# Optimization experiments

Measured on AMD Instinct MI355X. Metric: run time of the kernel, lower is better.

The kernel has to match this reference:

```python
import jax, jax.numpy as jnp
import numpy as np

T, B, E, H, R, NHASH, CHUNK = 2048, 2, 1024, 8, 2, 8, 32
D = E // H
INF = 1.0e16  # module's self.inf
BIG = 1.0e8   # module's self.big


def setup_inputs() -> dict:
    key = jax.random.key(0)
    ks = jax.random.split(key, 8)
    w = lambda k, shape, s=0.02: jax.random.normal(k, shape, dtype=jnp.float32) * s
    return {
        "query": jax.random.normal(ks[0], (T, B, E), jnp.float32),
        "key":   jax.random.normal(ks[1], (T, B, E), jnp.float32),
        "value": jax.random.normal(ks[2], (T, B, E), jnp.float32),
        "Wq": w(ks[3], (E, E)), "bq": jnp.zeros((E,), jnp.float32),
        "Wv": w(ks[4], (E, E)), "bv": jnp.zeros((E,), jnp.float32),
        "Wo": w(ks[5], (E, E)), "bo": jnp.zeros((E,), jnp.float32),
        "hash_w": w(ks[6], (R, H, D, NHASH // 2), 0.1),
    }


def _hashes(x_tbhd, hash_w):
    # einsum('ibnf,rnfh->ibrnh'), cat([lin,-lin]), argmax -> [T,B,R,H]
    lin = jnp.einsum('tbhd,rhdn->tbrhn', x_tbhd, hash_w)
    return jnp.argmax(jnp.concatenate([lin, -lin], axis=-1), axis=-1)


def _gather_t(x_bhtd, perm_brht):
    # gather along T with per-(b,r,h) permutation -> [B,R,H,T,D]
    Bb, Rr, Hh, Tt = perm_brht.shape
    Dd = x_bhtd.shape[-1]
    xb = jnp.broadcast_to(x_bhtd[:, None], (Bb, Rr, Hh, Tt, Dd))
    idx = jnp.broadcast_to(perm_brht[..., None], (Bb, Rr, Hh, Tt, Dd))
    return jnp.take_along_axis(xb, idx, axis=3)


def reference(query, key, value, Wq, bq, Wv, bv, Wo, bo, hash_w):
    del key  # share_kq=True (self-attention): keys are L2-normalized queries
    scaling = D ** -0.5
    qf = query @ Wq + bq                                    # [T,B,E]
    kf = qf / jnp.linalg.norm(qf, axis=-1, keepdims=True)   # F.normalize over embed dim
    vf = value @ Wv + bv
    q = qf.reshape(T, B, H, D) * scaling
    k = kf.reshape(T, B, H, D)
    v = vf.reshape(T, B, H, D)

    q_hash = _hashes(q, hash_w)                             # [T,B,R,H]
    k_hash = _hashes(k, hash_w)

    qh_t = jnp.transpose(q_hash, (1, 2, 3, 0))              # [B,R,H,T]
    kh_t = jnp.transpose(k_hash, (1, 2, 3, 0))
    p_q = jnp.argsort(qh_t, axis=-1)                        # stable sort by hash
    p_k = jnp.argsort(kh_t, axis=-1)
    inv_q = jnp.argsort(p_q, axis=-1)                       # sorted position of each token

    q_s = _gather_t(jnp.transpose(q, (1, 2, 0, 3)), p_q)    # [B,R,H,T,D]
    k_s = _gather_t(jnp.transpose(k, (1, 2, 0, 3)), p_k)
    v_s = _gather_t(jnp.transpose(v, (1, 2, 0, 3)), p_k)
    qh_s = jnp.take_along_axis(qh_t, p_q, axis=-1)
    kh_s = jnp.take_along_axis(kh_t, p_k, axis=-1)

    C = T // CHUNK
    M = 3 * CHUNK
    chunk = lambda x: x.reshape(x.shape[:3] + (C, CHUNK) + x.shape[4:])
    q_c, qh_c, qid_c = chunk(q_s), chunk(qh_s), chunk(p_q)
    k_c, v_c, kh_c, kid_c = chunk(k_s), chunk(v_s), chunk(kh_s), chunk(p_k)

    # each query chunk attends key chunks {c-1, c, c+1} (num_chunk_offsets=3, wraparound)
    blocks = lambda x: jnp.concatenate([jnp.roll(x, 1, axis=3), x, jnp.roll(x, -1, axis=3)], axis=4)
    kb, vb, khb, kidb = blocks(k_c), blocks(v_c), blocks(kh_c), blocks(kid_c)

    scores = jnp.einsum('brhcld,brhcmd->brhclm', q_c, kb)   # q pre-scaled by d^-0.5
    scores = scores - INF * (qh_c[..., :, None] != khb[..., None, :])   # mask_different_hashes
    scores = scores - BIG * (qid_c[..., :, None] == kidb[..., None, :]) # mask_current

    # cross-round duplicate counting: key ids attended per original query
    chunk_of = inv_q // CHUNK                               # [B,R,H,T]
    idx = jnp.broadcast_to(chunk_of[..., None], (B, R, H, T, M))
    A = jnp.take_along_axis(kidb, idx, axis=3)              # [B,R,H,T,M]
    dup = []
    for r in range(R):
        c = jnp.zeros((B, H, T, M), jnp.int32)
        for r2 in range(R):
            c = c + (A[:, r, :, :, :, None] == A[:, r2, :, :, None, :]).sum(-1, dtype=jnp.int32)
        dup.append(c)
    dup = jnp.stack(dup, axis=1)                            # [B,R,H,T,M]
    idx2 = jnp.broadcast_to(p_q[..., None], (B, R, H, T, M))
    dup_s = jnp.take_along_axis(dup, idx2, axis=3)          # sorted-query order
    scores = scores - jnp.log(dup_s.astype(scores.dtype)).reshape(scores.shape)

    z = jax.nn.logsumexp(scores, axis=-1)                   # [B,R,H,C,L]
    attn = jax.nn.softmax(scores, axis=-1)
    o = jnp.einsum('brhclm,brhcmd->brhcld', attn, vb).reshape(B, R, H, T, D)
    z = z.reshape(B, R, H, T)

    # scatter back to original token order
    idx3 = jnp.broadcast_to(inv_q[..., None], (B, R, H, T, D))
    o = jnp.take_along_axis(o, idx3, axis=3)
    z = jnp.take_along_axis(z, inv_q, axis=3)

    w = jax.nn.softmax(z, axis=1)                           # combine rounds by logsumexp weight
    out = (w[..., None] * o).sum(axis=1)                    # [B,H,T,D]
    out = jnp.transpose(out, (2, 0, 1, 3)).reshape(T, B, E)
    return out @ Wo + bo
```

## Files before the change

### kernel.cpp

```cpp
#include <hip/hip_runtime.h>

typedef unsigned short ushort_t;
typedef __bf16 bf16x8 __attribute__((ext_vector_type(8)));
typedef float f32x4 __attribute__((ext_vector_type(4)));

#define T_DIM 2048
#define B_DIM 2
#define E_DIM 1024
#define H_DIM 8
#define R_DIM 2
#define D_DIM 128
#define M_WIN 96
#define SCALING 0.08838834764831845f
#define LN2F 0.69314718055994530942f

__device__ __forceinline__ float bfu(unsigned u) {
  union { unsigned i; float f; } x; x.i = u << 16; return x.f;
}
__device__ __forceinline__ unsigned f2bf(float f) {
  union { float f; unsigned i; } x; x.f = f;
  unsigned r = x.i + 0x7fffu + ((x.i >> 16) & 1u);
  return r >> 16;
}
__device__ __forceinline__ void gl_lds16(const void* g, void* l) {
  __builtin_amdgcn_global_load_lds(
      (const __attribute__((address_space(1))) unsigned int*)g,
      (__attribute__((address_space(3))) unsigned int*)l, 16, 0, 0);
}

__global__ __launch_bounds__(256, 4) void prep2_kernel(
    const float* __restrict__ query, const float* __restrict__ value,
    const float* __restrict__ Wq, const float* __restrict__ Wv,
    const float* __restrict__ Wo, const float* __restrict__ bq,
    const float* __restrict__ hw,
    ushort_t* __restrict__ qh, ushort_t* __restrict__ vh,
    ushort_t* __restrict__ WqT, ushort_t* __restrict__ WvT,
    ushort_t* __restrict__ WoT, float* __restrict__ F,
    float* __restrict__ cvec, float* __restrict__ snorm)
{
  __shared__ float plds[4160];
  const int bid = blockIdx.x, tid = threadIdx.x;
  if (bid < 8192) {
    const float* src = (bid < 4096) ? query : value;
    ushort_t* dst = (bid < 4096) ? qh : vh;
    int i = ((bid & 4095) * 256 + tid) * 4;
    float4 x = *(const float4*)&src[i];
    uint2 oh;
    oh.x = f2bf(x.x) | (f2bf(x.y) << 16);
    oh.y = f2bf(x.z) | (f2bf(x.w) << 16);
    *(uint2*)&dst[i] = oh;
  } else if (bid < 8960) {
    int idx = bid - 8192;
    const float* in = (idx < 256) ? Wq : (idx < 512) ? Wv : Wo;
    ushort_t* hi = (idx < 256) ? WqT : (idx < 512) ? WvT : WoT;
    int tile = idx & 255;
    int n0 = (tile & 15) * 64, k0 = (tile >> 4) * 64;
    float (*t64)[65] = (float(*)[65])plds;
    const int tr = tid >> 4, tc4 = (tid & 15) * 4;
#pragma unroll
    for (int rr = 0; rr < 64; rr += 16)
      *(float4*)&t64[tr + rr][tc4] = *(const float4*)&in[(size_t)(k0 + tr + rr) * E_DIM + n0 + tc4];
    __syncthreads();
#pragma unroll
    for (int rr = 0; rr < 64; rr += 16) {
      int n = n0 + tr + rr;
      uint2 oh;
      oh.x = f2bf(t64[tc4 + 0][tr + rr]) | (f2bf(t64[tc4 + 1][tr + rr]) << 16);
      oh.y = f2bf(t64[tc4 + 2][tr + rr]) | (f2bf(t64[tc4 + 3][tr + rr]) << 16);
      *(uint2*)&hi[(size_t)n * E_DIM + k0 + tc4] = oh;
    }
  } else if (bid < 9024) {
    float* wl = plds;
    const int rh = (bid - 8960) & 15, h = rh & 7;
    const int e = ((bid - 8960) >> 4) * 256 + tid;
    for (int i = tid; i < 512; i += 256) wl[i] = hw[rh * 512 + i];
    __syncthreads();
    const float* wr = Wq + (size_t)e * E_DIM + h * D_DIM;
    float a0 = 0.f, a1 = 0.f, a2 = 0.f, a3 = 0.f;
#pragma unroll 2
    for (int d = 0; d < 128; d += 2) {
      float2 q2 = *(const float2*)&wr[d];
      float4 w0 = *(const float4*)&wl[d * 4];
      float4 w1 = *(const float4*)&wl[d * 4 + 4];
      a0 += q2.x * w0.x + q2.y * w1.x;
      a1 += q2.x * w0.y + q2.y * w1.y;
      a2 += q2.x * w0.z + q2.y * w1.z;
      a3 += q2.x * w0.w + q2.y * w1.w;
    }
    float4 o; o.x = a0; o.y = a1; o.z = a2; o.w = a3;
    *(float4*)&F[(size_t)e * 64 + rh * 4] = o;
    if ((bid - 8960) < 16 && tid < 4) {
      float acc = 0.f;
#pragma unroll 1
      for (int d = 0; d < 128; ++d) acc += bq[h * D_DIM + d] * wl[d * 4 + tid];
      cvec[rh * 4 + tid] = acc;
    }
  } else {
    float4 z4 = {0.f, 0.f, 0.f, 0.f};
#pragma unroll
    for (int i = 0; i < 4; ++i)
      *(float4*)&snorm[(i * 256 + tid) * 4] = z4;
  }
}

__global__ __launch_bounds__(256) void hashlin_kernel(const float* __restrict__ query,
                                                      const float* __restrict__ F,
                                                      const float* __restrict__ cvec,
                                                      int* __restrict__ hashb)
{
  __shared__ float As[32][17];
  __shared__ float Fs[32][64];
  const int tid = threadIdx.x;
  const int ty = tid >> 4, tx = tid & 15;
  const int r0 = blockIdx.x * 16;
  float acc0 = 0.f, acc1 = 0.f, acc2 = 0.f, acc3 = 0.f;
  for (int k0 = 0; k0 < E_DIM; k0 += 32) {
    __syncthreads();
    {
      int i = tid * 2, row = i >> 5, kk = i & 31;
      float2 a2 = *(const float2*)&query[(size_t)(r0 + row) * E_DIM + k0 + kk];
      As[kk][row] = a2.x; As[kk + 1][row] = a2.y;
    }
    {
      int i = tid * 8, kk = i >> 6, cc = i & 63;
      float4 f0 = *(const float4*)&F[(size_t)(k0 + kk) * 64 + cc];
      float4 f1 = *(const float4*)&F[(size_t)(k0 + kk) * 64 + cc + 4];
      *(float4*)&Fs[kk][cc] = f0;
      *(float4*)&Fs[kk][cc + 4] = f1;
    }
    __syncthreads();
#pragma unroll
    for (int kk = 0; kk < 32; ++kk) {
      float a = As[kk][ty];
      float4 f4 = *(const float4*)&Fs[kk][tx * 4];
      acc0 += a * f4.x; acc1 += a * f4.y; acc2 += a * f4.z; acc3 += a * f4.w;
    }
  }
  float4 c4 = *(const float4*)&cvec[tx * 4];
  float lin[4] = {acc0 + c4.x, acc1 + c4.y, acc2 + c4.z, acc3 + c4.w};
  float best = lin[0]; int bi = 0;
#pragma unroll
  for (int idx = 1; idx < 8; ++idx) {
    float v = (idx < 4) ? lin[idx] : -lin[idx - 4];
    if (v > best) { best = v; bi = idx; }
  }
  int grow = r0 + ty;
  int t = grow >> 1, b = grow & 1;
  int rr = tx >> 3, hh = tx & 7;
  hashb[(size_t)((b * R_DIM + rr) * H_DIM + hh) * T_DIM + t] = bi;
}

__global__ __launch_bounds__(256) void gemm_mfma(
    const ushort_t* __restrict__ A0, const ushort_t* __restrict__ B0,
    const float* __restrict__ bias0, ushort_t* __restrict__ Cb0, float* __restrict__ Cf0,
    const ushort_t* __restrict__ A1, const ushort_t* __restrict__ B1,
    const float* __restrict__ bias1, ushort_t* __restrict__ Cb1, float* __restrict__ Cf1,
    float* __restrict__ snorm, int do_norm)
{
  const ushort_t* Ah = blockIdx.z ? A1 : A0;
  const ushort_t* Bh = blockIdx.z ? B1 : B0;
  const float* bias = blockIdx.z ? bias1 : bias0;
  ushort_t* Cb = blockIdx.z ? Cb1 : Cb0;
  float* Cf = blockIdx.z ? Cf1 : Cf0;

  __shared__ ushort_t As[128 * 32];
  __shared__ ushort_t Bs[128 * 32];
  const int tid = threadIdx.x, w = tid >> 6, lane = tid & 63;
  const int lm = lane & 15, quad = lane >> 4;
  const int wr = w >> 1, wc = w & 1;
  const int m0 = blockIdx.y * 128, n0 = blockIdx.x * 128;
  const int lrow = lane >> 2, lcol = (lane & 3) * 8;

  f32x4 acc[4][4] = {};

  for (int k0 = 0; k0 < E_DIM; k0 += 32) {
    __syncthreads();
#pragma unroll
    for (int k = 0; k < 8; ++k) {
      if ((k & 3) == w) {
        gl_lds16(Ah + (size_t)(m0 + k * 16 + lrow) * E_DIM + k0 + lcol, &As[k * 512]);
        gl_lds16(Bh + (size_t)(n0 + k * 16 + lrow) * E_DIM + k0 + lcol, &Bs[k * 512]);
      }
    }
    __syncthreads();
    bf16x8 av[4], bv[4];
#pragma unroll
    for (int i = 0; i < 4; ++i) av[i] = *(const bf16x8*)&As[(wr * 64 + i * 16 + lm) * 32 + quad * 8];
#pragma unroll
    for (int j = 0; j < 4; ++j) bv[j] = *(const bf16x8*)&Bs[(wc * 64 + j * 16 + lm) * 32 + quad * 8];
#pragma unroll
    for (int i = 0; i < 4; ++i)
#pragma unroll
      for (int j = 0; j < 4; ++j)
        acc[i][j] = __builtin_amdgcn_mfma_f32_16x16x32_bf16(av[i], bv[j], acc[i][j], 0, 0, 0);
  }

  float rs[4][4] = {};
#pragma unroll
  for (int j = 0; j < 4; ++j) {
    int col = n0 + wc * 64 + j * 16 + lm;
    float bj = bias[col];
#pragma unroll
    for (int i = 0; i < 4; ++i) {
      int rowb = m0 + wr * 64 + i * 16 + quad * 4;
#pragma unroll
      for (int rg = 0; rg < 4; ++rg) {
        float val = acc[i][j][rg] + bj;
        if (Cb) {
          unsigned ub = f2bf(val);
          Cb[(size_t)(rowb + rg) * E_DIM + col] = (ushort_t)ub;
          float vb = bfu(ub);
          rs[i][rg] += vb * vb;
        } else {
          Cf[(size_t)(rowb + rg) * E_DIM + col] = val;
        }
      }
    }
  }
  if (do_norm && blockIdx.z == 0) {
#pragma unroll
    for (int i = 0; i < 4; ++i)
#pragma unroll
      for (int rg = 0; rg < 4; ++rg) {
        float s = rs[i][rg];
        s += __shfl_xor(s, 1);
        s += __shfl_xor(s, 2);
        s += __shfl_xor(s, 4);
        s += __shfl_xor(s, 8);
        if (lm == 0)
          atomicAdd(&snorm[m0 + wr * 64 + i * 16 + quad * 4 + rg], s);
      }
  }
}

__global__ __launch_bounds__(256) void sort_kernel(const int* __restrict__ hashb,
                                                   int* __restrict__ p, int* __restrict__ inv)
{
  const int bid = blockIdx.x, tid = threadIdx.x;
  const int lane = tid & 63, w = tid >> 6;
  const int* hrow = hashb + (size_t)bid * T_DIM;
  __shared__ int mat[8][256];
  __shared__ int btot[8], bbase[8];
  int cnt[8];
#pragma unroll
  for (int v = 0; v < 8; ++v) cnt[v] = 0;
  int hv[8];
#pragma unroll
  for (int j = 0; j < 8; ++j) { hv[j] = hrow[tid * 8 + j]; cnt[hv[j]]++; }
#pragma unroll
  for (int v = 0; v < 8; ++v) mat[v][tid] = cnt[v];
  __syncthreads();
  for (int v = w; v < 8; v += 4) {
    int4 c4 = *(const int4*)&mat[v][lane * 4];
    int s = c4.x + c4.y + c4.z + c4.w;
    int x = s;
    for (int off = 1; off < 64; off <<= 1) {
      int y = __shfl_up(x, off);
      if (lane >= off) x += y;
    }
    int excl = x - s;
    mat[v][lane * 4 + 0] = excl;
    mat[v][lane * 4 + 1] = excl + c4.x;
    mat[v][lane * 4 + 2] = excl + c4.x + c4.y;
    mat[v][lane * 4 + 3] = excl + c4.x + c4.y + c4.z;
    if (lane == 63) btot[v] = x;
  }
  __syncthreads();
  if (tid == 0) {
    int run = 0;
    for (int v = 0; v < 8; ++v) { bbase[v] = run; run += btot[v]; }
  }
  __syncthreads();
#pragma unroll
  for (int v = 0; v < 8; ++v) cnt[v] = 0;
#pragma unroll
  for (int j = 0; j < 8; ++j) {
    int v = hv[j];
    int pos = bbase[v] + mat[v][tid] + cnt[v];
    cnt[v]++;
    p[(size_t)bid * T_DIM + pos] = tid * 8 + j;
    inv[(size_t)bid * T_DIM + tid * 8 + j] = pos;
  }
}

__global__ __launch_bounds__(256) void gather_kernel(
    const ushort_t* __restrict__ qfb, const ushort_t* __restrict__ vfb,
    const float* __restrict__ snorm, const int* __restrict__ hashb,
    const int* __restrict__ p, const int* __restrict__ inv,
    int* __restrict__ meta_s, float* __restrict__ invn_s,
    ushort_t* __restrict__ ksort, ushort_t* __restrict__ vt)
{
  const int c = blockIdx.x, brh = blockIdx.y;
  const int b = brh >> 4, h = brh & 7;
  const int brh_o = brh ^ 8;
  const int tid = threadIdx.x;
  __shared__ int ts[32];
  __shared__ ushort_t vtile[32 * 136];

  if (tid < 32) {
    int pos = c * 32 + tid;
    int t = p[(size_t)brh * T_DIM + pos];
    int hh = hashb[(size_t)brh * T_DIM + t];
    int co = inv[(size_t)brh_o * T_DIM + t] >> 5;
    meta_s[(size_t)brh * T_DIM + pos] = t | (hh << 11) | (co << 14);
    invn_s[(size_t)brh * T_DIM + pos] = 1.0f / sqrtf(snorm[t * B_DIM + b]);
    ts[tid] = t;
  }
  __syncthreads();
  {
    int i = tid >> 3, part = tid & 7;
    int t = ts[i];
    const ushort_t* src = qfb + ((size_t)(t * B_DIM + b) << 10) + h * D_DIM + part * 16;
    uint4 a = *(const uint4*)src;
    uint4 bb = *(const uint4*)(src + 8);
    ushort_t* dst = ksort + ((size_t)brh * T_DIM + c * 32 + i) * 136 + part * 16;
    *(uint4*)dst = a; *(uint4*)(dst + 8) = bb;
    const ushort_t* vsrc = vfb + ((size_t)(t * B_DIM + b) << 10) + h * D_DIM + part * 16;
    uint4 va = *(const uint4*)vsrc;
    uint4 vb = *(const uint4*)(vsrc + 8);
    ushort_t* vdst = &vtile[i * 136 + part * 16];
    *(uint4*)vdst = va; *(uint4*)(vdst + 8) = vb;
  }
  __syncthreads();
  {
    int d = tid >> 1, half = tid & 1;
    unsigned pk[8];
#pragma unroll
    for (int jj = 0; jj < 8; ++jj) {
      unsigned lo = vtile[(half * 16 + jj * 2) * 136 + d];
      unsigned hi = vtile[(half * 16 + jj * 2 + 1) * 136 + d];
      pk[jj] = lo | (hi << 16);
    }
    ushort_t* out = vt + ((size_t)(brh * 64 + c)) * 4096 + d * 32 + half * 16;
    uint4 o0; o0.x = pk[0]; o0.y = pk[1]; o0.z = pk[2]; o0.w = pk[3];
    uint4 o1; o1.x = pk[4]; o1.y = pk[5]; o1.z = pk[6]; o1.w = pk[7];
    *(uint4*)out = o0; *(uint4*)(out + 8) = o1;
  }
}

__global__ __launch_bounds__(256) void attn_kernel(
    const ushort_t* __restrict__ ksort, const ushort_t* __restrict__ vt,
    const int* __restrict__ meta_s, const float* __restrict__ invn_s,
    ushort_t* __restrict__ o_out, float* __restrict__ z_out)
{
  const int c = blockIdx.x, h = blockIdx.y, bz = blockIdx.z;
  const int b = bz >> 1, r = bz & 1;
  const int brh = (b * R_DIM + r) * H_DIM + h;
  const int tid = threadIdx.x;
  const int lane = tid & 63, w = tid >> 6;
  const int lm = lane & 15, quad = lane >> 4;

  __shared__ __align__(16) unsigned char smem[50688];
  ushort_t* Kw = (ushort_t*)smem;
  ushort_t* VTb = (ushort_t*)(smem + 26112);
  float*    SS = (float*)smem;
  ushort_t* Ps = (ushort_t*)(smem + 13312);
  __shared__ int skp[M_WIN];
  __shared__ float s_invn[M_WIN];

  int cjs[3] = {(c + 63) & 63, c, (c + 1) & 63};

  int cnt = 0;
#pragma unroll
  for (int j = 0; j < 3; ++j) {
    const ushort_t* gk = ksort + ((size_t)brh * T_DIM + cjs[j] * 32) * 136;
    ushort_t* lk = Kw + j * 4352;
#pragma unroll
    for (int k = 0; k < 8; ++k) {
      if ((cnt++ & 3) == w) gl_lds16(gk + k * 512 + lane * 8, lk + k * 512);
    }
    if ((cnt++ & 3) == w) {
      if (lane < 32) gl_lds16(gk + 4096 + lane * 8, lk + 4096);
    }
  }
#pragma unroll
  for (int j = 0; j < 3; ++j) {
    const ushort_t* gv = vt + ((size_t)(brh * 64 + cjs[j])) * 4096;
    ushort_t* lv = VTb + j * 4096;
#pragma unroll
    for (int k = 0; k < 8; ++k) {
      if ((cnt++ & 3) == w) gl_lds16(gv + k * 512 + lane * 8, lv + k * 512);
    }
  }
  if (tid < M_WIN) {
    int pos = cjs[tid >> 5] * 32 + (tid & 31);
    skp[tid] = meta_s[(size_t)brh * T_DIM + pos];
    s_invn[tid] = invn_s[(size_t)brh * T_DIM + pos];
  }
  __syncthreads();

  const int mw = w & 1, nset = w >> 1;
  bf16x8 av[4];
#pragma unroll
  for (int kk = 0; kk < 4; ++kk)
    av[kk] = *(const bf16x8*)&Kw[(32 + mw * 16 + lm) * 136 + kk * 32 + quad * 8];
  f32x4 sacc[3] = {};
#pragma unroll
  for (int jj = 0; jj < 3; ++jj) {
    int nt = nset * 3 + jj;
#pragma unroll
    for (int kk = 0; kk < 4; ++kk) {
      bf16x8 bv = *(const bf16x8*)&Kw[(nt * 16 + lm) * 136 + kk * 32 + quad * 8];
      sacc[jj] = __builtin_amdgcn_mfma_f32_16x16x32_bf16(av[kk], bv, sacc[jj], 0, 0, 0);
    }
  }
  __syncthreads();

  const int rowb = mw * 16 + quad * 4;
#pragma unroll
  for (int jj = 0; jj < 3; ++jj) {
    int col = (nset * 3 + jj) * 16 + lm;
    int kp = skp[col];
    float scl = SCALING * s_invn[col];
#pragma unroll
    for (int rg = 0; rg < 4; ++rg) {
      int qp = skp[32 + rowb + rg];
      float sc = sacc[jj][rg] * scl;
      if ((kp ^ qp) & 0x3800) sc -= 1.0e16f;
      if (!((kp ^ qp) & 0x7FF)) sc -= 1.0e8f;
      int dc = ((kp >> 14) - (qp >> 14)) & 63;
      if (dc <= 1 || dc == 63) sc -= LN2F;
      SS[(rowb + rg) * 100 + col] = sc;
    }
  }
  __syncthreads();

  {
    const int l = tid >> 3, g = tid & 7;
    float smy[12];
#pragma unroll
    for (int j = 0; j < 12; ++j) smy[j] = SS[l * 100 + g + 8 * j];
    float mx = smy[0];
#pragma unroll
    for (int j = 1; j < 12; ++j) mx = fmaxf(mx, smy[j]);
    mx = fmaxf(mx, __shfl_xor(mx, 1));
    mx = fmaxf(mx, __shfl_xor(mx, 2));
    mx = fmaxf(mx, __shfl_xor(mx, 4));
    float sum = 0.f, ey[12];
#pragma unroll
    for (int j = 0; j < 12; ++j) { ey[j] = expf(smy[j] - mx); sum += ey[j]; }
    sum += __shfl_xor(sum, 1);
    sum += __shfl_xor(sum, 2);
    sum += __shfl_xor(sum, 4);
    float inv_s = 1.0f / sum;
#pragma unroll
    for (int j = 0; j < 12; ++j)
      Ps[l * 104 + g + 8 * j] = (ushort_t)f2bf(ey[j] * inv_s);
    if (g == 0) z_out[(size_t)brh * T_DIM + (skp[32 + l] & 2047)] = mx + logf(sum);
  }
  __syncthreads();

  const int dset = w >> 1;
  bf16x8 pa[3];
#pragma unroll
  for (int kk = 0; kk < 3; ++kk)
    pa[kk] = *(const bf16x8*)&Ps[(mw * 16 + lm) * 104 + kk * 32 + quad * 8];
  f32x4 oacc[4] = {};
#pragma unroll
  for (int jj = 0; jj < 4; ++jj) {
    int dt = dset * 4 + jj;
#pragma unroll
    for (int kk = 0; kk < 3; ++kk) {
      const ushort_t* VTk = VTb + kk * 4096;
      bf16x8 bv = *(const bf16x8*)&VTk[(dt * 16 + lm) * 32 + quad * 8];
      oacc[jj] = __builtin_amdgcn_mfma_f32_16x16x32_bf16(pa[kk], bv, oacc[jj], 0, 0, 0);
    }
  }
#pragma unroll
  for (int jj = 0; jj < 4; ++jj) {
    int col = (dset * 4 + jj) * 16 + lm;
#pragma unroll
    for (int rg = 0; rg < 4; ++rg) {
      int tqo = skp[32 + rowb + rg] & 2047;
      o_out[((size_t)brh * T_DIM + tqo) * D_DIM + col] = (ushort_t)f2bf(oacc[jj][rg]);
    }
  }
}

__global__ __launch_bounds__(256) void combine_kernel(const ushort_t* __restrict__ obf,
                                                      const float* __restrict__ z_buf,
                                                      ushort_t* __restrict__ ctx)
{
  int gid = blockIdx.x * 256 + threadIdx.x;
  int d4 = gid & 31;
  int t = (gid >> 5) & (T_DIM - 1);
  int h = (gid >> 16) & 7;
  int b = gid >> 19;
  int brh0 = (b * R_DIM + 0) * H_DIM + h;
  int brh1 = brh0 + H_DIM;
  float z0 = z_buf[(size_t)brh0 * T_DIM + t], z1 = z_buf[(size_t)brh1 * T_DIM + t];
  float mz = fmaxf(z0, z1);
  float e0 = expf(z0 - mz), e1 = expf(z1 - mz);
  float is = 1.0f / (e0 + e1);
  float w0 = e0 * is, w1 = e1 * is;
  uint2 a = *(const uint2*)&obf[((size_t)brh0 * T_DIM + t) * D_DIM + d4 * 4];
  uint2 cc = *(const uint2*)&obf[((size_t)brh1 * T_DIM + t) * D_DIM + d4 * 4];
  uint2 o;
  o.x = f2bf(w0 * bfu(a.x & 0xffffu) + w1 * bfu(cc.x & 0xffffu)) |
        (f2bf(w0 * bfu(a.x >> 16) + w1 * bfu(cc.x >> 16)) << 16);
  o.y = f2bf(w0 * bfu(a.y & 0xffffu) + w1 * bfu(cc.y & 0xffffu)) |
        (f2bf(w0 * bfu(a.y >> 16) + w1 * bfu(cc.y >> 16)) << 16);
  *(uint2*)&ctx[((size_t)(t * B_DIM + b) << 10) + h * D_DIM + d4 * 4] = o;
}

extern "C" void kernel_launch(void* const* d_in, const int* in_sizes, int n_in,
                              void* d_out, int out_size, void* d_ws, size_t ws_size,
                              hipStream_t stream)
{
  const float* query = (const float*)d_in[0];
  const float* value = (const float*)d_in[2];
  const float* Wq = (const float*)d_in[3];
  const float* bq = (const float*)d_in[4];
  const float* Wv = (const float*)d_in[5];
  const float* bv = (const float*)d_in[6];
  const float* Wo = (const float*)d_in[7];
  const float* bo = (const float*)d_in[8];
  const float* hw = (const float*)d_in[9];

  float* ws = (float*)d_ws;
  ushort_t* qh    = (ushort_t*)ws;
  ushort_t* vh    = qh + 4194304;
  ushort_t* obuf  = qh;
  ushort_t* qfb   = (ushort_t*)(ws + 4194304);
  ushort_t* ctx   = qfb;
  ushort_t* vfb   = qfb + 4194304;
  ushort_t* ksort = vfb + 4194304;
  ushort_t* vt    = ksort + 8912896;
  ushort_t* WqTh  = vt + 8388608;
  ushort_t* WvTh  = WqTh + 1048576;
  ushort_t* WoTh  = WvTh + 1048576;
  float* F        = (float*)(WoTh + 1048576);
  float* cvec     = F + 65536;
  float* zbuf     = cvec + 64;
  float* snorm    = zbuf + 65536;
  int* hashb      = (int*)(snorm + 4096);
  int* pperm      = hashb + 65536;
  int* pinv       = pperm + 65536;
  int* meta_s     = pinv + 65536;
  float* invn_s   = (float*)(meta_s + 65536);

  prep2_kernel<<<9025, 256, 0, stream>>>(query, value, Wq, Wv, Wo, bq, hw,
                                         qh, vh, WqTh, WvTh, WoTh, F, cvec, snorm);
  hashlin_kernel<<<256, 256, 0, stream>>>(query, F, cvec, hashb);
  gemm_mfma<<<dim3(8, 32, 2), 256, 0, stream>>>(qh, WqTh, bq, qfb, (float*)nullptr,
                                                vh, WvTh, bv, vfb, (float*)nullptr,
                                                snorm, 1);
  sort_kernel<<<32, 256, 0, stream>>>(hashb, pperm, pinv);
  gather_kernel<<<dim3(64, 32), 256, 0, stream>>>(qfb, vfb, snorm, hashb, pperm, pinv,
                                                  meta_s, invn_s, ksort, vt);
  attn_kernel<<<dim3(64, 8, 4), 256, 0, stream>>>(ksort, vt, meta_s, invn_s, obuf, zbuf);
  combine_kernel<<<4096, 256, 0, stream>>>(obuf, zbuf, ctx);
  gemm_mfma<<<dim3(8, 32, 1), 256, 0, stream>>>(ctx, WoTh, bo, (ushort_t*)nullptr, (float*)d_out,
                                                (const ushort_t*)nullptr, (const ushort_t*)nullptr,
                                                (const float*)nullptr, (ushort_t*)nullptr, (float*)nullptr,
                                                snorm, 0);
}
```

Measured before the change: 258.2 us.

## Split-K hash projection across waves and widen GEMM K-step to 64

The hash projection kernel now loads 128-wide K chunks and splits the K range across its four waves. Each thread computes a 4x4 register tile instead of a 1x4 strip, and the partial sums are reduced through shared memory before the argmax. The bf16 MFMA GEMM now stages two 32-wide K slices per iteration, which halves the number of barrier pairs per K loop. The cost is more shared memory per block (a reduction buffer in the hash kernel, doubled tiles in the GEMM), which may lower occupancy.

```diff
diff --git a/kernel.cpp b/kernel.cpp
--- a/kernel.cpp
+++ b/kernel.cpp
@@ -108,46 +108,80 @@
                                                       const float* __restrict__ cvec,
                                                       int* __restrict__ hashb)
 {
-  __shared__ float As[32][17];
-  __shared__ float Fs[32][64];
+  __shared__ float As[128 * 16];
+  __shared__ float Fs[128 * 64];
+  __shared__ float red[4 * 16 * 64];
   const int tid = threadIdx.x;
-  const int ty = tid >> 4, tx = tid & 15;
+  const int w = tid >> 6, lane = tid & 63;
+  const int ty = lane >> 4, tx = lane & 15;
   const int r0 = blockIdx.x * 16;
-  float acc0 = 0.f, acc1 = 0.f, acc2 = 0.f, acc3 = 0.f;
-  for (int k0 = 0; k0 < E_DIM; k0 += 32) {
+
+  float acc[4][4] = {};
+
+  for (int kc = 0; kc < E_DIM; kc += 128) {
     __syncthreads();
     {
-      int i = tid * 2, row = i >> 5, kk = i & 31;
-      float2 a2 = *(const float2*)&query[(size_t)(r0 + row) * E_DIM + k0 + kk];
-      As[kk][row] = a2.x; As[kk + 1][row] = a2.y;
+      int row = tid >> 4, kq = tid & 15;
+      const float* src = &query[(size_t)(r0 + row) * E_DIM + kc + kq * 8];
+      float4 a0 = *(const float4*)src;
+      float4 a1 = *(const float4*)(src + 4);
+      As[(kq * 8 + 0) * 16 + row] = a0.x; As[(kq * 8 + 1) * 16 + row] = a0.y;
+      As[(kq * 8 + 2) * 16 + row] = a0.z; As[(kq * 8 + 3) * 16 + row] = a0.w;
+      As[(kq * 8 + 4) * 16 + row] = a1.x; As[(kq * 8 + 5) * 16 + row] = a1.y;
+      As[(kq * 8 + 6) * 16 + row] = a1.z; As[(kq * 8 + 7) * 16 + row] = a1.w;
     }
     {
-      int i = tid * 8, kk = i >> 6, cc = i & 63;
-      float4 f0 = *(const float4*)&F[(size_t)(k0 + kk) * 64 + cc];
-      float4 f1 = *(const float4*)&F[(size_t)(k0 + kk) * 64 + cc + 4];
-      *(float4*)&Fs[kk][cc] = f0;
-      *(float4*)&Fs[kk][cc + 4] = f1;
+#pragma unroll
+      for (int u = 0; u < 4; ++u) {
+        int i = u * 2048 + tid * 8;
+        float4 f0 = *(const float4*)&F[(size_t)kc * 64 + i];
+        float4 f1 = *(const float4*)&F[(size_t)kc * 64 + i + 4];
+        *(float4*)&Fs[i] = f0;
+        *(float4*)&Fs[i + 4] = f1;
+      }
     }
     __syncthreads();
+    const int kbase = w * 32;
 #pragma unroll
     for (int kk = 0; kk < 32; ++kk) {
-      float a = As[kk][ty];
-      float4 f4 = *(const float4*)&Fs[kk][tx * 4];
-      acc0 += a * f4.x; acc1 += a * f4.y; acc2 += a * f4.z; acc3 += a * f4.w;
-    }
-  }
-  float4 c4 = *(const float4*)&cvec[tx * 4];
-  float lin[4] = {acc0 + c4.x, acc1 + c4.y, acc2 + c4.z, acc3 + c4.w};
-  float best = lin[0]; int bi = 0;
-#pragma unroll
-  for (int idx = 1; idx < 8; ++idx) {
-    float v = (idx < 4) ? lin[idx] : -lin[idx - 4];
-    if (v > best) { best = v; bi = idx; }
-  }
-  int grow = r0 + ty;
-  int t = grow >> 1, b = grow & 1;
-  int rr = tx >> 3, hh = tx & 7;
-  hashb[(size_t)((b * R_DIM + rr) * H_DIM + hh) * T_DIM + t] = bi;
+      float4 av = *(const float4*)&As[(kbase + kk) * 16 + ty * 4];
+      float4 fv = *(const float4*)&Fs[(kbase + kk) * 64 + tx * 4];
+      const float aa[4] = {av.x, av.y, av.z, av.w};
+      const float ff[4] = {fv.x, fv.y, fv.z, fv.w};
+#pragma unroll
+      for (int i = 0; i < 4; ++i)
+#pragma unroll
+        for (int j = 0; j < 4; ++j) acc[i][j] += aa[i] * ff[j];
+    }
+  }
+  __syncthreads();
+#pragma unroll
+  for (int i = 0; i < 4; ++i)
+#pragma unroll
+    for (int j = 0; j < 4; ++j)
+      red[(w * 16 + ty * 4 + i) * 64 + tx * 4 + j] = acc[i][j];
+  __syncthreads();
+  {
+    const int row = tid >> 4, rh = tid & 15;
+    float lin[4];
+#pragma unroll
+    for (int n = 0; n < 4; ++n) {
+      int col = rh * 4 + n;
+      lin[n] = red[(0 * 16 + row) * 64 + col] + red[(1 * 16 + row) * 64 + col] +
+               red[(2 * 16 + row) * 64 + col] + red[(3 * 16 + row) * 64 + col] +
+               cvec[col];
+    }
+    float best = lin[0]; int bi = 0;
+#pragma unroll
+    for (int idx = 1; idx < 8; ++idx) {
+      float v = (idx < 4) ? lin[idx] : -lin[idx - 4];
+      if (v > best) { best = v; bi = idx; }
+    }
+    int grow = r0 + row;
+    int t = grow >> 1, b = grow & 1;
+    int rr = rh >> 3, hh = rh & 7;
+    hashb[(size_t)((b * R_DIM + rr) * H_DIM + hh) * T_DIM + t] = bi;
+  }
 }
 
 __global__ __launch_bounds__(256) void gemm_mfma(
@@ -163,8 +197,8 @@
   ushort_t* Cb = blockIdx.z ? Cb1 : Cb0;
   float* Cf = blockIdx.z ? Cf1 : Cf0;
 
-  __shared__ ushort_t As[128 * 32];
-  __shared__ ushort_t Bs[128 * 32];
+  __shared__ ushort_t As[2][128 * 32];
+  __shared__ ushort_t Bs[2][128 * 32];
   const int tid = threadIdx.x, w = tid >> 6, lane = tid & 63;
   const int lm = lane & 15, quad = lane >> 4;
   const int wr = w >> 1, wc = w & 1;
@@ -173,26 +207,32 @@
 
   f32x4 acc[4][4] = {};
 
-  for (int k0 = 0; k0 < E_DIM; k0 += 32) {
+  for (int k0 = 0; k0 < E_DIM; k0 += 64) {
     __syncthreads();
 #pragma unroll
-    for (int k = 0; k < 8; ++k) {
-      if ((k & 3) == w) {
-        gl_lds16(Ah + (size_t)(m0 + k * 16 + lrow) * E_DIM + k0 + lcol, &As[k * 512]);
-        gl_lds16(Bh + (size_t)(n0 + k * 16 + lrow) * E_DIM + k0 + lcol, &Bs[k * 512]);
+    for (int s = 0; s < 2; ++s) {
+#pragma unroll
+      for (int k = 0; k < 8; ++k) {
+        if ((k & 3) == w) {
+          gl_lds16(Ah + (size_t)(m0 + k * 16 + lrow) * E_DIM + k0 + s * 32 + lcol, &As[s][k * 512]);
+          gl_lds16(Bh + (size_t)(n0 + k * 16 + lrow) * E_DIM + k0 + s * 32 + lcol, &Bs[s][k * 512]);
+        }
       }
     }
     __syncthreads();
-    bf16x8 av[4], bv[4];
-#pragma unroll
-    for (int i = 0; i < 4; ++i) av[i] = *(const bf16x8*)&As[(wr * 64 + i * 16 + lm) * 32 + quad * 8];
-#pragma unroll
-    for (int j = 0; j < 4; ++j) bv[j] = *(const bf16x8*)&Bs[(wc * 64 + j * 16 + lm) * 32 + quad * 8];
-#pragma unroll
-    for (int i = 0; i < 4; ++i)
-#pragma unroll
-      for (int j = 0; j < 4; ++j)
-        acc[i][j] = __builtin_amdgcn_mfma_f32_16x16x32_bf16(av[i], bv[j], acc[i][j], 0, 0, 0);
+#pragma unroll
+    for (int s = 0; s < 2; ++s) {
+      bf16x8 av[4], bv[4];
+#pragma unroll
+      for (int i = 0; i < 4; ++i) av[i] = *(const bf16x8*)&As[s][(wr * 64 + i * 16 + lm) * 32 + quad * 8];
+#pragma unroll
+      for (int j = 0; j < 4; ++j) bv[j] = *(const bf16x8*)&Bs[s][(wc * 64 + j * 16 + lm) * 32 + quad * 8];
+#pragma unroll
+      for (int i = 0; i < 4; ++i)
+#pragma unroll
+        for (int j = 0; j < 4; ++j)
+          acc[i][j] = __builtin_amdgcn_mfma_f32_16x16x32_bf16(av[i], bv[j], acc[i][j], 0, 0, 0);
+    }
   }
 
   float rs[4][4] = {};
```

Result: faster. 241.6 us (-6.5%).
